# Performance work log

Measured on AMD Instinct MI355X. Metric: run time of the kernel, lower is better.

Reference implementation:

```python
import jax, jax.numpy as jnp
import numpy as np

EPS = 1e-6

def _layer_norm(x, w, b):
    mu = jnp.mean(x, axis=-1, keepdims=True)
    var = jnp.mean((x - mu) ** 2, axis=-1, keepdims=True)
    return (x - mu) * jax.lax.rsqrt(var + EPS) * w + b

def setup_inputs() -> dict:
    key = jax.random.key(0)
    ks = jax.random.split(key, 8)
    B, N, C = 4, 1024, 2048
    H = C * 2  # mlp hidden = 2*feature_dim
    std = 0.01
    x = jax.random.normal(ks[0], (B, N, C), dtype=jnp.float32)
    wq = jax.random.normal(ks[1], (C, C), dtype=jnp.float32) * std
    wk = jax.random.normal(ks[2], (C, C), dtype=jnp.float32) * std
    wv = jax.random.normal(ks[3], (C, C), dtype=jnp.float32) * std
    ln1_w = jnp.ones((C,), jnp.float32); ln1_b = jnp.zeros((C,), jnp.float32)
    fc1_w = jax.random.normal(ks[4], (H, C), dtype=jnp.float32) * std
    fc1_b = jnp.zeros((H,), jnp.float32)
    fc2_w = jax.random.normal(ks[5], (C, H), dtype=jnp.float32) * std
    fc2_b = jnp.zeros((C,), jnp.float32)
    ln2_w = jnp.ones((C,), jnp.float32); ln2_b = jnp.zeros((C,), jnp.float32)
    return {"x": x, "wq": wq, "wk": wk, "wv": wv,
            "ln1_w": ln1_w, "ln1_b": ln1_b,
            "fc1_w": fc1_w, "fc1_b": fc1_b,
            "fc2_w": fc2_w, "fc2_b": fc2_b,
            "ln2_w": ln2_w, "ln2_b": ln2_b}

def reference(x, wq, wk, wv, ln1_w, ln1_b, fc1_w, fc1_b, fc2_w, fc2_b, ln2_w, ln2_b):
    B, N, C = x.shape
    num_head = 32
    d = C // num_head
    # QKV projections (no bias), split heads: [B, H, N, d]
    def proj(w):
        return (x @ w.T).reshape(B, N, num_head, d).transpose(0, 2, 1, 3)
    q, k, v = proj(wq), proj(wk), proj(wv)
    scale = 1.0 / jnp.sqrt(jnp.float32(d))
    attn = jnp.einsum('bhnd,bhmd->bhnm', q * scale, k)
    attn = jax.nn.softmax(attn, axis=-1)
    out = jnp.einsum('bhnm,bhmd->bhnd', attn, v)
    out = out.transpose(0, 2, 1, 3).reshape(B, N, C)
    out = _layer_norm(out + x, ln1_w, ln1_b)
    # MLP with residual + post-LN
    h = jax.nn.relu(out @ fc1_w.T + fc1_b)
    h = h @ fc2_w.T + fc2_b
    out = _layer_norm(out + h, ln2_w, ln2_b)
    return out
```

## Files before the change

kernel.cpp:

```cpp
#include <hip/hip_runtime.h>

#define C_DIM   2048
#define H_DIM   4096
#define NSEQ    1024
#define NBATCH  4
#define BN_ROWS 4096
#define NHEAD   32
#define DHEAD   64

typedef __attribute__((ext_vector_type(8))) short  short8;
typedef __attribute__((ext_vector_type(4))) float  f32x4;

__device__ __forceinline__ float bf2f(unsigned short u) {
    union { unsigned int i; float f; } v; v.i = ((unsigned int)u) << 16; return v.f;
}
__device__ __forceinline__ unsigned short f2bf(float f) {
    union { float f; unsigned int i; } v; v.f = f;
    unsigned int r = v.i + 0x7fffu + ((v.i >> 16) & 1u);
    return (unsigned short)(r >> 16);
}

#define G2L16(gp, lp) \
    __builtin_amdgcn_global_load_lds((const __attribute__((address_space(1))) void*)(gp), \
                                     (__attribute__((address_space(3))) void*)(lp), 16, 0, 0)

__global__ __launch_bounds__(256)
void cvt_all(const float* __restrict__ x,   unsigned short* __restrict__ xo,
             const float* __restrict__ w0,  unsigned short* __restrict__ w0o,
             const float* __restrict__ w1,  unsigned short* __restrict__ w1o,
             const float* __restrict__ w2,  unsigned short* __restrict__ w2o,
             const float* __restrict__ w3,  unsigned short* __restrict__ w3o,
             const float* __restrict__ w4,  unsigned short* __restrict__ w4o)
{
    int bid = blockIdx.x;
    const float* src; unsigned short* dst;
    if      (bid < 2048) { src = x;  dst = xo;  }
    else if (bid < 3072) { src = w0; dst = w0o; bid -= 2048; }
    else if (bid < 4096) { src = w1; dst = w1o; bid -= 3072; }
    else if (bid < 5120) { src = w2; dst = w2o; bid -= 4096; }
    else if (bid < 7168) { src = w3; dst = w3o; bid -= 5120; }
    else                 { src = w4; dst = w4o; bid -= 7168; }
    const size_t i = ((size_t)bid * 256 + threadIdx.x) * 16;
    #pragma unroll
    for (int h = 0; h < 2; ++h) {
        float4 a = *(const float4*)(src + i + h * 8);
        float4 b = *(const float4*)(src + i + h * 8 + 4);
        unsigned short o[8] = { f2bf(a.x), f2bf(a.y), f2bf(a.z), f2bf(a.w),
                                f2bf(b.x), f2bf(b.y), f2bf(b.z), f2bf(b.w) };
        *(int4*)(dst + i + h * 8) = *(const int4*)o;
    }
}

__global__ __launch_bounds__(256)
void gemm_qkv(const unsigned short* __restrict__ A,
              const unsigned short* __restrict__ Wq,
              const unsigned short* __restrict__ Wk,
              const unsigned short* __restrict__ Wv,
              unsigned short* __restrict__ Qo,
              unsigned short* __restrict__ Ko,
              unsigned short* __restrict__ Vo)
{
    __shared__ unsigned short As[128 * 32];
    __shared__ unsigned short Bs[128 * 32];

    const int t    = threadIdx.x;
    const int lane = t & 63;
    const int wave = t >> 6;

    const int hwid = blockIdx.x + blockIdx.y * 32;
    const int swz  = (hwid & 7) * 192 + (hwid >> 3);
    const int m0   = (swz / 48) * 128;
    const int ng   = (swz % 48) * 128;

    const unsigned short* B; unsigned short* Cp; int n0;
    if      (ng < 2048) { B = Wq; Cp = Qo; n0 = ng; }
    else if (ng < 4096) { B = Wk; Cp = Ko; n0 = ng - 2048; }
    else                { B = Wv; Cp = Vo; n0 = ng - 4096; }

    const int wm = (wave >> 1) * 64, wn = (wave & 1) * 64;
    const int lr = lane & 15;
    const int kq = lane >> 4;

    f32x4 acc[4][4] = {};

    const int lrow = lane >> 2;
    const int lcol = (lane & 3) * 8;

    for (int kt = 0; kt < C_DIM; kt += 32) {
        __syncthreads();
        #pragma unroll
        for (int p = 0; p < 2; ++p) {
            const int rb = wave * 32 + p * 16;
            G2L16(&A[(size_t)(m0 + rb + lrow) * C_DIM + kt + lcol], &As[rb * 32]);
            G2L16(&B[(size_t)(n0 + rb + lrow) * C_DIM + kt + lcol], &Bs[rb * 32]);
        }
        __syncthreads();

        short8 af[4], bf[4];
        #pragma unroll
        for (int i = 0; i < 4; ++i)
            af[i] = *(const short8*)&As[(wm + i * 16 + lr) * 32 + kq * 8];
        #pragma unroll
        for (int j = 0; j < 4; ++j)
            bf[j] = *(const short8*)&Bs[(wn + j * 16 + lr) * 32 + kq * 8];
        #pragma unroll
        for (int i = 0; i < 4; ++i)
            #pragma unroll
            for (int j = 0; j < 4; ++j)
                acc[i][j] = __builtin_amdgcn_mfma_f32_16x16x32_bf16(af[i], bf[j], acc[i][j], 0, 0, 0);
    }

    #pragma unroll
    for (int j = 0; j < 4; ++j) {
        const int col = n0 + wn + j * 16 + lr;
        #pragma unroll
        for (int i = 0; i < 4; ++i) {
            #pragma unroll
            for (int r = 0; r < 4; ++r) {
                const int row = m0 + wm + i * 16 + kq * 4 + r;
                Cp[(size_t)row * C_DIM + col] = f2bf(acc[i][j][r]);
            }
        }
    }
}

template<int EPI>
__device__ __forceinline__
void gemm256_body(const unsigned short* __restrict__ A,
                  const unsigned short* __restrict__ B,
                  const float* __restrict__ bias,
                  unsigned short* __restrict__ C,
                  const int m0, const int n0, const int K, const int ldc)
{
    __shared__ unsigned short As[2][256 * 64];
    __shared__ unsigned short Bs[2][256 * 64];

    const int t  = threadIdx.x;
    const int l  = t & 63;
    const int w  = t >> 6;
    const int wr = w >> 2;
    const int wc = w & 3;
    const int lr = l & 15;
    const int kq = l >> 4;
    const int slotA = lr & 7;

    const int sr = l >> 3;
    const int sg = ((l & 7) ^ sr) * 8;

    f32x4 acc[8][4] = {};
    short8 bf[4][2], af[2][2];

#define STG(src, srow0, ktile, ldsdst) do {                                         \
    const unsigned short* gp0_ = (src) + (size_t)((srow0) + w * 8 + sr) * K         \
                                  + (ktile) * 64 + sg;                              \
    const unsigned short* gp1_ = (src) + (size_t)((srow0) + 64 + w * 8 + sr) * K    \
                                  + (ktile) * 64 + sg;                              \
    G2L16(gp0_, (ldsdst) + (w * 8) * 64);                                           \
    G2L16(gp1_, (ldsdst) + (64 + w * 8) * 64);                                      \
  } while (0)

#define LDB(buf) do {                                                               \
    _Pragma("unroll") for (int n_ = 0; n_ < 4; ++n_)                                \
      _Pragma("unroll") for (int ks_ = 0; ks_ < 2; ++ks_)                           \
        bf[n_][ks_] = *(const short8*)&Bs[buf][                                     \
            (wc * 64 + n_ * 16 + lr) * 64 + (((ks_ << 2) | kq) ^ slotA) * 8];       \
  } while (0)

#define LDA(buf, q) do {                                                            \
    _Pragma("unroll") for (int i_ = 0; i_ < 2; ++i_)                                \
      _Pragma("unroll") for (int ks_ = 0; ks_ < 2; ++ks_)                           \
        af[i_][ks_] = *(const short8*)&As[buf][                                     \
            (wr * 128 + ((q) * 2 + i_) * 16 + lr) * 64                              \
            + (((ks_ << 2) | kq) ^ slotA) * 8];                                     \
  } while (0)

#define MM(q) do {                                                                  \
    __builtin_amdgcn_s_setprio(1);                                                  \
    _Pragma("unroll") for (int i_ = 0; i_ < 2; ++i_)                                \
      _Pragma("unroll") for (int n_ = 0; n_ < 4; ++n_)                              \
        _Pragma("unroll") for (int ks_ = 0; ks_ < 2; ++ks_)                         \
          acc[(q) * 2 + i_][n_] = __builtin_amdgcn_mfma_f32_16x16x32_bf16(          \
              af[i_][ks_], bf[n_][ks_], acc[(q) * 2 + i_][n_], 0, 0, 0);            \
    __builtin_amdgcn_s_setprio(0);                                                  \
  } while (0)

#define BARR() __builtin_amdgcn_s_barrier()
#define WLG0() asm volatile("s_waitcnt lgkmcnt(0)" ::: "memory")

    const int NT = K >> 6;
    const int IT = NT >> 1;

    STG(B, n0,       0, &Bs[0][0]);
    STG(B, n0 + 128, 0, &Bs[0][128 * 64]);
    STG(A, m0,       0, &As[0][0]);
    STG(A, m0 + 128, 0, &As[0][128 * 64]);
    STG(B, n0,       1, &Bs[1][0]);
    STG(B, n0 + 128, 1, &Bs[1][128 * 64]);
    asm volatile("s_waitcnt vmcnt(4)" ::: "memory");
    BARR();

    for (int it = 0; it < IT; ++it) {
        const int T1 = 2 * it + 1, T2 = 2 * it + 2, T3 = 2 * it + 3;
        const bool haveT2 = (T2 < NT), haveT3 = (T3 < NT);

        LDB(0); LDA(0, 0);
        STG(A, m0, T1, &As[1][0]);
        BARR(); WLG0(); MM(0); BARR();

        LDA(0, 1);
        STG(A, m0 + 128, T1, &As[1][128 * 64]);
        BARR(); WLG0(); MM(1); BARR();

        LDA(0, 2);
        if (haveT2) STG(B, n0, T2, &Bs[0][0]);
        BARR(); WLG0(); MM(2); BARR();

        LDA(0, 3);
        if (haveT2) STG(B, n0 + 128, T2, &Bs[0][128 * 64]);
        BARR(); WLG0(); MM(3);
        if (haveT2) asm volatile("s_waitcnt vmcnt(4)" ::: "memory");
        else        asm volatile("s_waitcnt vmcnt(0)" ::: "memory");
        BARR();

        LDB(1); LDA(1, 0);
        if (haveT2) STG(A, m0, T2, &As[0][0]);
        BARR(); WLG0(); MM(0); BARR();

        LDA(1, 1);
        if (haveT2) STG(A, m0 + 128, T2, &As[0][128 * 64]);
        BARR(); WLG0(); MM(1); BARR();

        LDA(1, 2);
        if (haveT3) STG(B, n0, T3, &Bs[1][0]);
        BARR(); WLG0(); MM(2); BARR();

        LDA(1, 3);
        if (haveT3) STG(B, n0 + 128, T3, &Bs[1][128 * 64]);
        BARR(); WLG0(); MM(3);
        if (it + 1 < IT) asm volatile("s_waitcnt vmcnt(4)" ::: "memory");
        BARR();
    }

    #pragma unroll
    for (int n = 0; n < 4; ++n) {
        const int col = n0 + wc * 64 + n * 16 + lr;
        float bv = 0.f;
        if (EPI > 0) bv = bias[col];
        #pragma unroll
        for (int m = 0; m < 8; ++m) {
            #pragma unroll
            for (int r = 0; r < 4; ++r) {
                const int row = m0 + wr * 128 + m * 16 + kq * 4 + r;
                float v = acc[m][n][r] + bv;
                if (EPI == 1) v = fmaxf(v, 0.f);
                C[(size_t)row * ldc + col] = f2bf(v);
            }
        }
    }
#undef STG
#undef LDB
#undef LDA
#undef MM
#undef BARR
#undef WLG0
}

__global__ __launch_bounds__(512, 2)
void gemm256_fc1(const unsigned short* __restrict__ A,
                 const unsigned short* __restrict__ B,
                 const float* __restrict__ bias,
                 unsigned short* __restrict__ C)
{
    const int hwid = blockIdx.x + blockIdx.y * 16;
    const int swz  = (hwid & 7) * 32 + (hwid >> 3);
    gemm256_body<1>(A, B, bias, C, (swz >> 4) * 256, (swz & 15) * 256, C_DIM, H_DIM);
}

template<int EPI, typename OUT_T>
__global__ __launch_bounds__(256)
void gemm_ring(const unsigned short* __restrict__ A,
               const unsigned short* __restrict__ B,
               const float* __restrict__ bias,
               OUT_T* __restrict__ C, int M, int N, int K)
{
    __shared__ unsigned short As[4][128 * 32];
    __shared__ unsigned short Bs[4][128 * 32];

    const int t    = threadIdx.x;
    const int lane = t & 63;
    const int wave = t >> 6;

    const int nwgy = gridDim.y;
    const int nwg  = gridDim.x * nwgy;
    const int hwid = blockIdx.x + blockIdx.y * gridDim.x;
    const int swz  = (hwid & 7) * (nwg >> 3) + (hwid >> 3);
    const int m0 = (swz / nwgy) * 128, n0 = (swz % nwgy) * 128;

    const int wm = (wave >> 1) * 64, wn = (wave & 1) * 64;
    const int lr = lane & 15;
    const int kq = lane >> 4;
    const int lrow = lane >> 2;
    const int lcol = (lane & 3) * 8;
    const int NT = K >> 5;

    const int arow = m0 + wave * 32 + lrow;
    const int brow = n0 + wave * 32 + lrow;
    const int rb   = wave * 32;

    f32x4 acc[4][4] = {};

#define STAGE_T(slot, ktile) do {                                              \
    const int koff_ = (ktile) * 32 + lcol;                                     \
    G2L16(&A[(size_t)(arow)      * K + koff_], &As[slot][ rb       * 32]);     \
    G2L16(&A[(size_t)(arow + 16) * K + koff_], &As[slot][(rb + 16) * 32]);     \
    G2L16(&B[(size_t)(brow)      * K + koff_], &Bs[slot][ rb       * 32]);     \
    G2L16(&B[(size_t)(brow + 16) * K + koff_], &Bs[slot][(rb + 16) * 32]);     \
  } while (0)

    STAGE_T(0, 0);
    STAGE_T(1, 1);
    STAGE_T(2, 2);

    for (int kt = 0; kt < NT; ++kt) {
        if (kt < NT - 2)       asm volatile("s_waitcnt vmcnt(8)" ::: "memory");
        else if (kt == NT - 2) asm volatile("s_waitcnt vmcnt(4)" ::: "memory");
        else                   asm volatile("s_waitcnt vmcnt(0)" ::: "memory");
        __builtin_amdgcn_s_barrier();

        const int s = kt & 3;
        short8 af[4], bfr[4];
        #pragma unroll
        for (int i = 0; i < 4; ++i)
            af[i] = *(const short8*)&As[s][(wm + i * 16 + lr) * 32 + kq * 8];
        #pragma unroll
        for (int j = 0; j < 4; ++j)
            bfr[j] = *(const short8*)&Bs[s][(wn + j * 16 + lr) * 32 + kq * 8];
        #pragma unroll
        for (int i = 0; i < 4; ++i)
            #pragma unroll
            for (int j = 0; j < 4; ++j)
                acc[i][j] = __builtin_amdgcn_mfma_f32_16x16x32_bf16(af[i], bfr[j], acc[i][j], 0, 0, 0);

        if (kt + 3 < NT) STAGE_T((kt + 3) & 3, kt + 3);
    }

    #pragma unroll
    for (int j = 0; j < 4; ++j) {
        const int col = n0 + wn + j * 16 + lr;
        float bv = 0.f;
        if (EPI > 0) bv = bias[col];
        #pragma unroll
        for (int i = 0; i < 4; ++i) {
            #pragma unroll
            for (int r = 0; r < 4; ++r) {
                const int row = m0 + wm + i * 16 + kq * 4 + r;
                float v = acc[i][j][r] + bv;
                if (EPI == 1) v = fmaxf(v, 0.f);
                if constexpr (sizeof(OUT_T) == 2) C[(size_t)row * N + col] = f2bf(v);
                else                              C[(size_t)row * N + col] = v;
            }
        }
    }
#undef STAGE_T
}

#define LDK 72
__global__ __launch_bounds__(256)
void attn_mfma(const unsigned short* __restrict__ Qg,
               const unsigned short* __restrict__ Kg,
               const unsigned short* __restrict__ Vg,
               unsigned short* __restrict__ Og)
{
    __shared__ unsigned short Ks[64 * LDK];
    __shared__ unsigned short Vt[64 * LDK];
    __shared__ unsigned short Ps[64 * LDK];

    const int t    = threadIdx.x;
    const int lane = t & 63;
    const int wave = t >> 6;
    const int lr   = lane & 15;
    const int quad = lane >> 4;
    const int bh = blockIdx.y;
    const int b  = bh >> 5, h = bh & 31;
    const int q0 = blockIdx.x * 64;
    const int colbase = h * 64;

    short8 qf[2];
    {
        const size_t qrow = (size_t)(b * NSEQ + q0 + wave * 16 + lr) * C_DIM + colbase;
        #pragma unroll
        for (int kc = 0; kc < 2; ++kc) {
            short8 raw = *(const short8*)(Qg + qrow + kc * 32 + quad * 8);
            short8 sc;
            #pragma unroll
            for (int j = 0; j < 8; ++j)
                sc[j] = (short)f2bf(bf2f((unsigned short)raw[j]) * 0.125f);
            qf[kc] = sc;
        }
    }

    f32x4 Oacc[4] = {};
    float li[4] = {};

    for (int kt = 0; kt < 16; ++kt) {
        __syncthreads();
        {
            const int r = t >> 2, sg = (t & 3) * 16;
            const size_t grow = (size_t)(b * NSEQ + kt * 64 + r) * C_DIM + colbase + sg;
            *(int4*)&Ks[r * LDK + sg]     = *(const int4*)(Kg + grow);
            *(int4*)&Ks[r * LDK + sg + 8] = *(const int4*)(Kg + grow + 8);
        }
        {
            const int key = t & 63, d0 = (t >> 6) * 16;
            const size_t grow = (size_t)(b * NSEQ + kt * 64 + key) * C_DIM + colbase + d0;
            int4 u0 = *(const int4*)(Vg + grow);
            int4 u1 = *(const int4*)(Vg + grow + 8);
            const unsigned short* us0 = (const unsigned short*)&u0;
            const unsigned short* us1 = (const unsigned short*)&u1;
            #pragma unroll
            for (int j = 0; j < 8; ++j) {
                Vt[(d0 + j)     * LDK + key] = us0[j];
                Vt[(d0 + j + 8) * LDK + key] = us1[j];
            }
        }
        __syncthreads();

        f32x4 s[4] = {};
        #pragma unroll
        for (int n = 0; n < 4; ++n)
            #pragma unroll
            for (int kc = 0; kc < 2; ++kc) {
                short8 kf = *(const short8*)&Ks[(n * 16 + lr) * LDK + kc * 32 + quad * 8];
                s[n] = __builtin_amdgcn_mfma_f32_16x16x32_bf16(qf[kc], kf, s[n], 0, 0, 0);
            }

        float p[4][4];
        #pragma unroll
        for (int r = 0; r < 4; ++r) {
            #pragma unroll
            for (int n = 0; n < 4; ++n) { p[n][r] = __expf(s[n][r]); }
            li[r] += p[0][r] + p[1][r] + p[2][r] + p[3][r];
        }

        #pragma unroll
        for (int r = 0; r < 4; ++r)
            #pragma unroll
            for (int n = 0; n < 4; ++n)
                Ps[(wave * 16 + quad * 4 + r) * LDK + n * 16 + lr] = f2bf(p[n][r]);

        short8 pf[2];
        #pragma unroll
        for (int kc = 0; kc < 2; ++kc)
            pf[kc] = *(const short8*)&Ps[(wave * 16 + lr) * LDK + kc * 32 + quad * 8];

        #pragma unroll
        for (int n = 0; n < 4; ++n)
            #pragma unroll
            for (int kc = 0; kc < 2; ++kc) {
                short8 vf = *(const short8*)&Vt[(n * 16 + lr) * LDK + kc * 32 + quad * 8];
                Oacc[n] = __builtin_amdgcn_mfma_f32_16x16x32_bf16(pf[kc], vf, Oacc[n], 0, 0, 0);
            }
    }

    #pragma unroll
    for (int r = 0; r < 4; ++r) {
        #pragma unroll
        for (int off = 1; off < 16; off <<= 1) li[r] += __shfl_xor(li[r], off, 64);
        const float inv = 1.f / li[r];
        const size_t rowb = (size_t)(b * NSEQ + q0 + wave * 16 + quad * 4 + r) * C_DIM + colbase;
        #pragma unroll
        for (int n = 0; n < 4; ++n)
            Og[rowb + n * 16 + lr] = f2bf(Oacc[n][r] * inv);
    }
}

__global__ __launch_bounds__(256)
void ln_fused1(const unsigned short* __restrict__ a, const float* __restrict__ xr,
               const float* __restrict__ w, const float* __restrict__ bb,
               unsigned short* __restrict__ y16)
{
    const int row = blockIdx.x, t = threadIdx.x;
    const size_t base = (size_t)row * C_DIM;
    const int c0 = t * 8;
    float v[8];
    int4 ai = *(const int4*)(a + base + c0);
    const unsigned short* as = (const unsigned short*)&ai;
    float4 x0 = *(const float4*)(xr + base + c0);
    float4 x1 = *(const float4*)(xr + base + c0 + 4);
    v[0] = bf2f(as[0]) + x0.x; v[1] = bf2f(as[1]) + x0.y;
    v[2] = bf2f(as[2]) + x0.z; v[3] = bf2f(as[3]) + x0.w;
    v[4] = bf2f(as[4]) + x1.x; v[5] = bf2f(as[5]) + x1.y;
    v[6] = bf2f(as[6]) + x1.z; v[7] = bf2f(as[7]) + x1.w;

    float s = 0.f, s2 = 0.f;
    #pragma unroll
    for (int k = 0; k < 8; ++k) { s += v[k]; s2 += v[k] * v[k]; }
    #pragma unroll
    for (int off = 32; off; off >>= 1) { s += __shfl_xor(s, off, 64); s2 += __shfl_xor(s2, off, 64); }
    __shared__ float red[8];
    if ((t & 63) == 0) { red[t >> 6] = s; red[4 + (t >> 6)] = s2; }
    __syncthreads();
    s  = red[0] + red[1] + red[2] + red[3];
    s2 = red[4] + red[5] + red[6] + red[7];
    const float mu = s * (1.f / C_DIM);
    const float rs = rsqrtf(s2 * (1.f / C_DIM) - mu * mu + 1e-6f);

    float4 w0 = *(const float4*)(w + c0);
    float4 w1 = *(const float4*)(w + c0 + 4);
    float4 b0 = *(const float4*)(bb + c0);
    float4 b1 = *(const float4*)(bb + c0 + 4);
    const float* wf = (const float*)&w0; const float* wg = (const float*)&w1;
    const float* bf = (const float*)&b0; const float* bg = (const float*)&b1;
    unsigned short o16[8];
    #pragma unroll
    for (int k = 0; k < 4; ++k) {
        o16[k]     = f2bf((v[k]     - mu) * rs * wf[k] + bf[k]);
        o16[k + 4] = f2bf((v[k + 4] - mu) * rs * wg[k] + bg[k]);
    }
    *(int4*)(y16 + base + c0) = *(const int4*)o16;
}

__global__ __launch_bounds__(256)
void ln_fused2(const unsigned short* __restrict__ a, const unsigned short* __restrict__ b2,
               const float* __restrict__ w, const float* __restrict__ bb,
               float* __restrict__ out)
{
    const int row = blockIdx.x, t = threadIdx.x;
    const size_t base = (size_t)row * C_DIM;
    const int c0 = t * 8;
    float v[8];
    int4 ai = *(const int4*)(a + base + c0);
    int4 bi = *(const int4*)(b2 + base + c0);
    const unsigned short* as = (const unsigned short*)&ai;
    const unsigned short* bs = (const unsigned short*)&bi;
    #pragma unroll
    for (int k = 0; k < 8; ++k) v[k] = bf2f(as[k]) + bf2f(bs[k]);

    float s = 0.f, s2 = 0.f;
    #pragma unroll
    for (int k = 0; k < 8; ++k) { s += v[k]; s2 += v[k] * v[k]; }
    #pragma unroll
    for (int off = 32; off; off >>= 1) { s += __shfl_xor(s, off, 64); s2 += __shfl_xor(s2, off, 64); }
    __shared__ float red[8];
    if ((t & 63) == 0) { red[t >> 6] = s; red[4 + (t >> 6)] = s2; }
    __syncthreads();
    s  = red[0] + red[1] + red[2] + red[3];
    s2 = red[4] + red[5] + red[6] + red[7];
    const float mu = s * (1.f / C_DIM);
    const float rs = rsqrtf(s2 * (1.f / C_DIM) - mu * mu + 1e-6f);

    float4 w0 = *(const float4*)(w + c0);
    float4 w1 = *(const float4*)(w + c0 + 4);
    float4 b0 = *(const float4*)(bb + c0);
    float4 b1 = *(const float4*)(bb + c0 + 4);
    const float* wf = (const float*)&w0; const float* wg = (const float*)&w1;
    const float* bf = (const float*)&b0; const float* bg = (const float*)&b1;
    float4 o0, o1;
    #pragma unroll
    for (int k = 0; k < 4; ++k) {
        ((float*)&o0)[k] = (v[k]     - mu) * rs * wf[k] + bf[k];
        ((float*)&o1)[k] = (v[k + 4] - mu) * rs * wg[k] + bg[k];
    }
    *(float4*)(out + base + c0)     = o0;
    *(float4*)(out + base + c0 + 4) = o1;
}

extern "C" void kernel_launch(void* const* d_in, const int* in_sizes, int n_in,
                              void* d_out, int out_size, void* d_ws, size_t ws_size,
                              hipStream_t stream)
{
    (void)in_sizes; (void)n_in; (void)out_size; (void)ws_size;
    const float* x    = (const float*)d_in[0];
    const float* wq   = (const float*)d_in[1];
    const float* wk   = (const float*)d_in[2];
    const float* wv   = (const float*)d_in[3];
    const float* ln1w = (const float*)d_in[4];
    const float* ln1b = (const float*)d_in[5];
    const float* fc1w = (const float*)d_in[6];
    const float* fc1b = (const float*)d_in[7];
    const float* fc2w = (const float*)d_in[8];
    const float* fc2b = (const float*)d_in[9];
    const float* ln2w = (const float*)d_in[10];
    const float* ln2b = (const float*)d_in[11];

    char* ws = (char*)d_ws;
    const size_t MB16 = (size_t)BN_ROWS * C_DIM * 2;
    unsigned short* xb    = (unsigned short*)(ws);
    unsigned short* attnb = (unsigned short*)(ws);
    unsigned short* wqb   = (unsigned short*)(ws + MB16);
    unsigned short* wkb   = (unsigned short*)(ws + MB16 + MB16 / 2);
    unsigned short* y16   = (unsigned short*)(ws + MB16);
    unsigned short* wvb   = (unsigned short*)(ws + 2 * MB16);
    unsigned short* fc1wb = (unsigned short*)(ws + 2 * MB16 + MB16 / 2);
    unsigned short* fc2wb = (unsigned short*)(ws + 3 * MB16 + MB16 / 2);
    unsigned short* q_ws  = (unsigned short*)(ws + 4 * MB16 + MB16 / 2);
    unsigned short* h2    = (unsigned short*)(ws + 4 * MB16 + MB16 / 2);
    unsigned short* k_ws  = (unsigned short*)(ws + 5 * MB16 + MB16 / 2);
    unsigned short* v_ws  = (unsigned short*)(ws + 6 * MB16 + MB16 / 2);
    unsigned short* hbuf  = (unsigned short*)(ws + 5 * MB16 + MB16 / 2);

    dim3 blk(256);

    cvt_all<<<dim3(9216), blk, 0, stream>>>(x, xb, wq, wqb, wk, wkb, wv, wvb,
                                            fc1w, fc1wb, fc2w, fc2wb);

    gemm_qkv<<<dim3(32, 48), blk, 0, stream>>>(xb, wqb, wkb, wvb, q_ws, k_ws, v_ws);
    attn_mfma<<<dim3(NSEQ / 64, NBATCH * NHEAD), blk, 0, stream>>>(q_ws, k_ws, v_ws, attnb);
    ln_fused1<<<dim3(BN_ROWS), blk, 0, stream>>>(attnb, x, ln1w, ln1b, y16);
    gemm256_fc1<<<dim3(16, 16), dim3(512), 0, stream>>>(y16, fc1wb, fc1b, hbuf);
    gemm_ring<2, unsigned short><<<dim3(32, 16), blk, 0, stream>>>(hbuf, fc2wb, fc2b, h2, BN_ROWS, C_DIM, H_DIM);
    ln_fused2<<<dim3(BN_ROWS), blk, 0, stream>>>(y16, h2, ln2w, ln2b, (float*)d_out);
}
```

Before: 565.4 us.

## Prefetch next K/V tile into registers in attention; drop GEMM block swizzle

Result: faster. 548.7 us (-3.0%).

```diff
diff --git a/kernel.cpp b/kernel.cpp
--- a/kernel.cpp
+++ b/kernel.cpp
@@ -66,12 +66,8 @@
     const int t    = threadIdx.x;
     const int lane = t & 63;
     const int wave = t >> 6;
-
-    const int hwid = blockIdx.x + blockIdx.y * 32;
-    const int swz  = (hwid & 7) * 192 + (hwid >> 3);
-    const int m0   = (swz / 48) * 128;
-    const int ng   = (swz % 48) * 128;
-
+    const int m0 = blockIdx.x * 128;
+    const int ng = blockIdx.y * 128;
     const unsigned short* B; unsigned short* Cp; int n0;
     if      (ng < 2048) { B = Wq; Cp = Qo; n0 = ng; }
     else if (ng < 4096) { B = Wk; Cp = Ko; n0 = ng - 2048; }
@@ -271,9 +267,7 @@
                  const float* __restrict__ bias,
                  unsigned short* __restrict__ C)
 {
-    const int hwid = blockIdx.x + blockIdx.y * 16;
-    const int swz  = (hwid & 7) * 32 + (hwid >> 3);
-    gemm256_body<1>(A, B, bias, C, (swz >> 4) * 256, (swz & 15) * 256, C_DIM, H_DIM);
+    gemm256_body<1>(A, B, bias, C, blockIdx.x * 256, blockIdx.y * 256, C_DIM, H_DIM);
 }
 
 template<int EPI, typename OUT_T>
@@ -289,13 +283,7 @@
     const int t    = threadIdx.x;
     const int lane = t & 63;
     const int wave = t >> 6;
-
-    const int nwgy = gridDim.y;
-    const int nwg  = gridDim.x * nwgy;
-    const int hwid = blockIdx.x + blockIdx.y * gridDim.x;
-    const int swz  = (hwid & 7) * (nwg >> 3) + (hwid >> 3);
-    const int m0 = (swz / nwgy) * 128, n0 = (swz % nwgy) * 128;
-
+    const int m0 = blockIdx.x * 128, n0 = blockIdx.y * 128;
     const int wm = (wave >> 1) * 64, wn = (wave & 1) * 64;
     const int lr = lane & 15;
     const int kq = lane >> 4;
@@ -399,29 +387,42 @@
         }
     }
 
+    const int r_k   = t >> 2, sg_k = (t & 3) * 16;
+    const int key_v = t & 63, d0_v = (t >> 6) * 16;
+    const size_t base_bh = (size_t)(b * NSEQ) * C_DIM + colbase;
+    int4 k0, k1, v0, v1;
+    {
+        const size_t gk = base_bh + (size_t)r_k * C_DIM + sg_k;
+        k0 = *(const int4*)(Kg + gk);
+        k1 = *(const int4*)(Kg + gk + 8);
+        const size_t gv = base_bh + (size_t)key_v * C_DIM + d0_v;
+        v0 = *(const int4*)(Vg + gv);
+        v1 = *(const int4*)(Vg + gv + 8);
+    }
+
     f32x4 Oacc[4] = {};
     float li[4] = {};
 
     for (int kt = 0; kt < 16; ++kt) {
         __syncthreads();
+        *(int4*)&Ks[r_k * LDK + sg_k]     = k0;
+        *(int4*)&Ks[r_k * LDK + sg_k + 8] = k1;
         {
-            const int r = t >> 2, sg = (t & 3) * 16;
-            const size_t grow = (size_t)(b * NSEQ + kt * 64 + r) * C_DIM + colbase + sg;
-            *(int4*)&Ks[r * LDK + sg]     = *(const int4*)(Kg + grow);
-            *(int4*)&Ks[r * LDK + sg + 8] = *(const int4*)(Kg + grow + 8);
-        }
-        {
-            const int key = t & 63, d0 = (t >> 6) * 16;
-            const size_t grow = (size_t)(b * NSEQ + kt * 64 + key) * C_DIM + colbase + d0;
-            int4 u0 = *(const int4*)(Vg + grow);
-            int4 u1 = *(const int4*)(Vg + grow + 8);
-            const unsigned short* us0 = (const unsigned short*)&u0;
-            const unsigned short* us1 = (const unsigned short*)&u1;
+            const unsigned short* us0 = (const unsigned short*)&v0;
+            const unsigned short* us1 = (const unsigned short*)&v1;
             #pragma unroll
             for (int j = 0; j < 8; ++j) {
-                Vt[(d0 + j)     * LDK + key] = us0[j];
-                Vt[(d0 + j + 8) * LDK + key] = us1[j];
+                Vt[(d0_v + j)     * LDK + key_v] = us0[j];
+                Vt[(d0_v + j + 8) * LDK + key_v] = us1[j];
             }
+        }
+        if (kt + 1 < 16) {
+            const size_t gk = base_bh + (size_t)((kt + 1) * 64 + r_k) * C_DIM + sg_k;
+            k0 = *(const int4*)(Kg + gk);
+            k1 = *(const int4*)(Kg + gk + 8);
+            const size_t gv = base_bh + (size_t)((kt + 1) * 64 + key_v) * C_DIM + d0_v;
+            v0 = *(const int4*)(Vg + gv);
+            v1 = *(const int4*)(Vg + gv + 8);
         }
         __syncthreads();
 
```
